# Kernel tuning notes

Measured on AMD Instinct MI355X. Metric: run time of the kernel, lower is better.

Reference implementation:

```python
import jax, jax.numpy as jnp
import numpy as np

L = 3          # num_layer
E_DIM = 64     # emb_dim
B = 4          # graphs per batch
N = 20000      # nodes per graph
E = 320000     # edges per graph
IN_DIM = 21    # raw node feature dim (Linear(21, emb_dim))
BN_EPS = 1e-5


def setup_inputs() -> dict:
    key = jax.random.key(0)
    ks = jax.random.split(key, 16)
    h2 = 2 * E_DIM
    inp = {
        "x": jax.random.normal(ks[0], (B, N, IN_DIM), dtype=jnp.float32),
        "edge_index": jax.random.randint(ks[1], (B, 2, E), 0, N, dtype=jnp.int64),
        "edge_attr": jax.random.normal(ks[2], (B, E, 1), dtype=jnp.float32),
        # layer-0 input node embedding Linear(21, emb)
        "inW": jax.random.normal(ks[3], (IN_DIM, E_DIM), dtype=jnp.float32) * 0.1,
        "inb": jnp.zeros((E_DIM,), dtype=jnp.float32),
        # per-layer edge encoder Linear(1, emb)
        "edgeW": jax.random.normal(ks[4], (L, 1, E_DIM), dtype=jnp.float32) * 0.1,
        "edgeb": jnp.zeros((L, E_DIM), dtype=jnp.float32),
        # per-layer MLP: Linear(2e,2e) -> BN(2e) -> ReLU -> Linear(2e,e)
        "W1": jax.random.normal(ks[5], (L, h2, h2), dtype=jnp.float32) * 0.05,
        "b1": jnp.zeros((L, h2), dtype=jnp.float32),
        "gamma": jnp.ones((L, h2), dtype=jnp.float32),
        "beta": jnp.zeros((L, h2), dtype=jnp.float32),
        "W2": jax.random.normal(ks[6], (L, h2, E_DIM), dtype=jnp.float32) * 0.05,
        "b2": jnp.zeros((L, E_DIM), dtype=jnp.float32),
    }
    return inp


def _batchnorm_train(h, g, b):
    # BatchNorm1d in training mode: per-graph stats over the node dim, biased var
    m = h.mean(axis=0)
    v = jnp.mean((h - m) ** 2, axis=0)
    return (h - m) * jax.lax.rsqrt(v + BN_EPS) * g + b


def _gin_layer(xg, eig, eag, W1l, b1l, gl, bel, W2l, b2l):
    # xg [N,e], eig [2,E], eag [E,e]
    x_j = xg[eig[0]]                                   # gather source nodes [E,e]
    msg = jnp.concatenate([x_j, eag], axis=-1)         # [E,2e]
    aggr = jax.ops.segment_sum(msg, eig[1], num_segments=N)  # scatter-add [N,2e]
    h = aggr @ W1l + b1l
    h = _batchnorm_train(h, gl, bel)
    h = jax.nn.relu(h)
    return h @ W2l + b2l                               # [N,e]


def reference(x, edge_index, edge_attr, inW, inb, edgeW, edgeb, W1, b1, gamma, beta, W2, b2):
    h = x
    for l in range(L):
        ea = edge_attr @ edgeW[l] + edgeb[l]           # [B,E,e] edge embeddings
        if l == 0:
            h = h @ inW + inb                          # [B,N,e]
        h = jax.vmap(_gin_layer, in_axes=(0, 0, 0, None, None, None, None, None, None))(
            h, edge_index, ea, W1[l], b1[l], gamma[l], beta[l], W2[l], b2[l])
        if l < L - 1:                                  # drop_ratio=0 -> dropout is identity
            h = jax.nn.relu(h)
    return h  # JK='last'
```

## Files before the change

### kernel.cpp

```cpp
#include <hip/hip_runtime.h>
#include <hip/hip_bf16.h>
#include <hip/hip_fp16.h>

#define NB 4
#define NN 20000
#define NE 320000
#define IND 21
#define ED 64
#define H2 128
#define CAP 48
#define NRANGE 32
#define RNODES 625
#define BINCAP 160
#define SCAP 11264
#define BN_EPS 1e-5f

typedef __attribute__((ext_vector_type(8))) short bf16x8;
typedef __attribute__((ext_vector_type(4))) float f32x4;

__device__ __forceinline__ short f2bf(float f) {
    unsigned u = __float_as_uint(f);
    u += 0x7fffu + ((u >> 16) & 1u);
    return (short)(u >> 16);
}

__device__ __forceinline__ void add8(float* ac, const uint4 rv) {
    const float2 f0 = __half22float2(*(const __half2*)&rv.x);
    const float2 f1 = __half22float2(*(const __half2*)&rv.y);
    const float2 f2 = __half22float2(*(const __half2*)&rv.z);
    const float2 f3 = __half22float2(*(const __half2*)&rv.w);
    ac[0] += f0.x; ac[1] += f0.y; ac[2] += f1.x; ac[3] += f1.y;
    ac[4] += f2.x; ac[5] += f2.y; ac[6] += f3.x; ac[7] += f3.y;
}


__global__ __launch_bounds__(256) void k_compact(
    const int* __restrict__ ei, const float* __restrict__ eattr,
    uint2* __restrict__ stage, int* __restrict__ rcnt)
{
    __shared__ uint2 bins[NRANGE][BINCAP];
    __shared__ int lcnt[NRANGE];
    __shared__ int lbase[NRANGE];
    const int b = blockIdx.y;
    const int e0 = blockIdx.x * 2048;
    const int tid = threadIdx.x;
    if (tid < NRANGE) lcnt[tid] = 0;
    __syncthreads();
    const int* srcp = ei + (size_t)b * 2 * NE;
    const int* dstp = srcp + NE;
    const float* ap = eattr + (size_t)b * NE;
    #pragma unroll
    for (int it = 0; it < 8; ++it) {
        const int e = e0 + it * 256 + tid;
        if (e < NE) {
            const int dst = dstp[e];
            const int src = srcp[e];
            const float a = ap[e];
            const int r = dst / RNODES;
            const unsigned lo = ((unsigned)src & 0xffffu) | (__float_as_uint(a) & 0xffff0000u);
            const int p = atomicAdd(&lcnt[r], 1);
            if (p < BINCAP) bins[r][p] = make_uint2(lo, (unsigned)dst);
        }
    }
    __syncthreads();
    if (tid < NRANGE) lbase[tid] = atomicAdd(&rcnt[b * NRANGE + tid], min(lcnt[tid], BINCAP));
    __syncthreads();
    for (int r = 0; r < NRANGE; ++r) {
        const int c = min(lcnt[r], BINCAP);
        uint2* dstg = stage + (size_t)(b * NRANGE + r) * SCAP + lbase[r];
        for (int i = tid; i < c; i += 256) dstg[i] = bins[r][i];
    }
}

__global__ __launch_bounds__(256) void k_scatter(
    const uint2* __restrict__ stage, const int* __restrict__ rcnt,
    int* __restrict__ cnt, unsigned int* __restrict__ bucket)
{
    const int b = blockIdx.x >> 5;
    const int g = blockIdx.x & 31;
    const int count = min(rcnt[b * NRANGE + g], SCAP);
    const uint2* st = stage + (size_t)(b * NRANGE + g) * SCAP;
    for (int idx = threadIdx.x; idx < count; idx += 256) {
        const uint2 rec = st[idx];
        const int node = b * NN + (int)rec.y;
        const int p = atomicAdd(&cnt[node], 1);
        if (p < CAP) bucket[(size_t)node * CAP + p] = rec.x;
    }
}

__global__ __launch_bounds__(256) void k_in(
    const float* __restrict__ x, const float* __restrict__ inW,
    const float* __restrict__ inb, __half* __restrict__ h)
{
    const int b = blockIdx.y;
    const int t = blockIdx.x * 256 + threadIdx.x;
    const int n = t >> 6;
    const int c = t & 63;
    if (n >= NN) return;
    const float* xr = x + ((size_t)b * NN + n) * IND;
    float acc = inb[c];
    #pragma unroll
    for (int k = 0; k < IND; ++k) acc += xr[k] * inW[k * ED + c];
    h[((size_t)b * NN + n) * ED + c] = __float2half(acc);
}

__global__ __launch_bounds__(256) void k_prep(
    const float* __restrict__ W1, const float* __restrict__ W2,
    const float* __restrict__ edgeW, const float* __restrict__ edgeb,
    short* __restrict__ W1T, short* __restrict__ W2T,
    float* __restrict__ uv_all, float* __restrict__ stats_all)
{
    const int l = blockIdx.x;
    const int tid = threadIdx.x;
    ((float4*)(stats_all + l * 1024))[tid] = make_float4(0.f, 0.f, 0.f, 0.f);
    for (int i = tid; i < H2 * ED; i += 256) {
        const int j = i >> 6, k = i & 63;
        W1T[l * 8192 + i] = f2bf(W1[(size_t)l * H2 * H2 + k * H2 + j]);
    }
    for (int i = tid; i < ED * H2; i += 256) {
        const int c = i >> 7, k = i & 127;
        W2T[l * 8192 + i] = f2bf(W2[(size_t)l * H2 * ED + k * ED + c]);
    }
    if (tid < H2) {
        float u = 0.f, v = 0.f;
        for (int k = 0; k < ED; ++k) {
            const float w = W1[(size_t)l * H2 * H2 + (ED + k) * H2 + tid];
            u += edgeW[l * ED + k] * w;
            v += edgeb[l * ED + k] * w;
        }
        uv_all[l * 256 + tid] = u;
        uv_all[l * 256 + H2 + tid] = v;
    }
}


__global__ __launch_bounds__(256, 4) void k_aggr_stats(
    const __half* __restrict__ h, const unsigned int* __restrict__ bucket,
    const int* __restrict__ cnt_arr, const short* __restrict__ W1Tl,
    const float* __restrict__ b1l, const float* __restrict__ uv_l,
    __half* __restrict__ h1g, float* __restrict__ stats_l)
{
    __shared__ short atb[16 * 72];
    __shared__ float sdl[16], ddl[16];
    __shared__ float uL[H2], vL[H2], bbL[H2];
    const int tid = threadIdx.x;
    const int g = blockIdx.x & 7;
    const int b = g >> 1;
    const int t = ((int)blockIdx.x >> 3) * 2 + (g & 1);
    const int n0 = t * 16;

    if (tid < H2) { uL[tid] = uv_l[tid]; vL[tid] = uv_l[H2 + tid]; bbL[tid] = b1l[tid]; }

    {
        const int node = n0 + (tid >> 4);
        const int sub = tid & 15;
        const int q = sub & 7;
        const int par = sub >> 3;
        const int cntraw = cnt_arr[b * NN + node];
        const int cnt = min(cntraw, CAP);
        const unsigned int* row = bucket + (size_t)(b * NN + node) * CAP;
        const __half* hp = h + (size_t)b * NN * ED + q * 8;
        float ac[8];
        #pragma unroll
        for (int i = 0; i < 8; ++i) ac[i] = 0.f;
        float sa = 0.f;
        const int nq = cnt >> 2;
        int qq = par;
        for (; qq + 2 < nq; qq += 4) {
            const uint4 sA = *(const uint4*)(row + qq * 4);
            const uint4 sB = *(const uint4*)(row + (qq + 2) * 4);
            const uint4 r0 = *(const uint4*)(hp + (size_t)(sA.x & 0xffffu) * ED);
            const uint4 r1 = *(const uint4*)(hp + (size_t)(sA.y & 0xffffu) * ED);
            const uint4 r2 = *(const uint4*)(hp + (size_t)(sA.z & 0xffffu) * ED);
            const uint4 r3 = *(const uint4*)(hp + (size_t)(sA.w & 0xffffu) * ED);
            const uint4 r4 = *(const uint4*)(hp + (size_t)(sB.x & 0xffffu) * ED);
            const uint4 r5 = *(const uint4*)(hp + (size_t)(sB.y & 0xffffu) * ED);
            const uint4 r6 = *(const uint4*)(hp + (size_t)(sB.z & 0xffffu) * ED);
            const uint4 r7 = *(const uint4*)(hp + (size_t)(sB.w & 0xffffu) * ED);
            sa += __uint_as_float(sA.x & 0xffff0000u) + __uint_as_float(sA.y & 0xffff0000u)
                + __uint_as_float(sA.z & 0xffff0000u) + __uint_as_float(sA.w & 0xffff0000u)
                + __uint_as_float(sB.x & 0xffff0000u) + __uint_as_float(sB.y & 0xffff0000u)
                + __uint_as_float(sB.z & 0xffff0000u) + __uint_as_float(sB.w & 0xffff0000u);
            add8(ac, r0); add8(ac, r1); add8(ac, r2); add8(ac, r3);
            add8(ac, r4); add8(ac, r5); add8(ac, r6); add8(ac, r7);
        }
        for (; qq < nq; qq += 2) {
            const uint4 sA = *(const uint4*)(row + qq * 4);
            const uint4 r0 = *(const uint4*)(hp + (size_t)(sA.x & 0xffffu) * ED);
            const uint4 r1 = *(const uint4*)(hp + (size_t)(sA.y & 0xffffu) * ED);
            const uint4 r2 = *(const uint4*)(hp + (size_t)(sA.z & 0xffffu) * ED);
            const uint4 r3 = *(const uint4*)(hp + (size_t)(sA.w & 0xffffu) * ED);
            sa += __uint_as_float(sA.x & 0xffff0000u) + __uint_as_float(sA.y & 0xffff0000u)
                + __uint_as_float(sA.z & 0xffff0000u) + __uint_as_float(sA.w & 0xffff0000u);
            add8(ac, r0); add8(ac, r1); add8(ac, r2); add8(ac, r3);
        }
        if ((nq & 1) == par) {
            for (int p = nq * 4; p < cnt; ++p) {
                const unsigned e = row[p];
                sa += __uint_as_float(e & 0xffff0000u);
                const uint4 r0 = *(const uint4*)(hp + (size_t)(e & 0xffffu) * ED);
                add8(ac, r0);
            }
        }
        #pragma unroll
        for (int i = 0; i < 8; ++i) ac[i] += __shfl_xor(ac[i], 8);
        sa += __shfl_xor(sa, 8);
        if (par == 0) {
            uint4 pk;
            pk.x = (unsigned short)f2bf(ac[0]) | ((unsigned int)(unsigned short)f2bf(ac[1]) << 16);
            pk.y = (unsigned short)f2bf(ac[2]) | ((unsigned int)(unsigned short)f2bf(ac[3]) << 16);
            pk.z = (unsigned short)f2bf(ac[4]) | ((unsigned int)(unsigned short)f2bf(ac[5]) << 16);
            pk.w = (unsigned short)f2bf(ac[6]) | ((unsigned int)(unsigned short)f2bf(ac[7]) << 16);
            *(uint4*)&atb[(tid >> 4) * 72 + q * 8] = pk;
            if (q == 0) {
                sdl[tid >> 4] = sa;
                ddl[tid >> 4] = (float)cntraw;
            }
        }
    }
    __syncthreads();

    const int l = tid & 63;
    const int w = tid >> 6;
    const int m = l & 15, quad = l >> 4;
    const int jb = w * 2;
    f32x4 acc[2];
    acc[0] = (f32x4){0.f, 0.f, 0.f, 0.f};
    acc[1] = (f32x4){0.f, 0.f, 0.f, 0.f};
    #pragma unroll
    for (int kc = 0; kc < 2; ++kc) {
        const bf16x8 fa = *(const bf16x8*)&atb[m * 72 + kc * 32 + quad * 8];
        #pragma unroll
        for (int t2 = 0; t2 < 2; ++t2) {
            const bf16x8 fb = *(const bf16x8*)&W1Tl[((jb + t2) * 16 + m) * 64 + kc * 32 + quad * 8];
            acc[t2] = __builtin_amdgcn_mfma_f32_16x16x32_bf16(fa, fb, acc[t2], 0, 0, 0);
        }
    }
    float sa_r[4], dg_r[4];
    #pragma unroll
    for (int r = 0; r < 4; ++r) {
        const int row = quad * 4 + r;
        sa_r[r] = sdl[row]; dg_r[r] = ddl[row];
    }
    #pragma unroll
    for (int t2 = 0; t2 < 2; ++t2) {
        const int j = (jb + t2) * 16 + m;
        const float u = uL[j], v = vL[j], bb = bbL[j];
        float ls = 0.f, lq = 0.f;
        #pragma unroll
        for (int r = 0; r < 4; ++r) {
            const float h1v = acc[t2][r] + sa_r[r] * u + dg_r[r] * v + bb;
            h1g[((size_t)b * NN + n0 + quad * 4 + r) * H2 + j] = __float2half(h1v);
            ls += h1v; lq += h1v * h1v;
        }
        ls += __shfl_xor(ls, 16); ls += __shfl_xor(ls, 32);
        lq += __shfl_xor(lq, 16); lq += __shfl_xor(lq, 32);
        if (l < 16) {
            atomicAdd(&stats_l[b * H2 + j], ls);
            atomicAdd(&stats_l[NB * H2 + b * H2 + j], lq);
        }
    }
}

__global__ __launch_bounds__(256) void k_mlp_out(
    const __half* __restrict__ h1g, const short* __restrict__ W2Tl,
    const float* __restrict__ stats_l, const float* __restrict__ gamma_l,
    const float* __restrict__ beta_l, const float* __restrict__ b2l,
    __half* __restrict__ outh, float* __restrict__ outf, int last)
{
    __shared__ short wt[ED * 136];
    __shared__ short pb[64 * 136];
    const int tid = threadIdx.x;
    const int g = blockIdx.x & 7;
    const int b = g >> 1;
    const int t = ((int)blockIdx.x >> 3) * 2 + (g & 1);
    if (t >= (NN + 63) / 64) return;
    const int n0 = t * 64;

    const uint4* h1p = (const uint4*)(h1g + ((size_t)b * NN + n0) * H2);
    const uint4 hv0 = h1p[tid];
    const uint4 hv1 = h1p[tid + 256];
    const uint4 hv2 = h1p[tid + 512];
    const uint4 hv3 = h1p[tid + 768];

    for (int i = tid; i < 1024; i += 256)
        *(uint4*)&wt[(i >> 4) * 136 + (i & 15) * 8] = ((const uint4*)W2Tl)[i];

    const int ch0 = (tid & 15) * 8;
    float sc[8], sh[8];
    #pragma unroll
    for (int e = 0; e < 8; ++e) {
        const int j = ch0 + e;
        const float mm = stats_l[b * H2 + j] * (1.f / NN);
        const float var = fmaxf(stats_l[NB * H2 + b * H2 + j] * (1.f / NN) - mm * mm, 0.f);
        const float rs = rsqrtf(var + BN_EPS);
        sc[e] = gamma_l[j] * rs;
        sh[e] = beta_l[j] - mm * sc[e];
    }

    {
        uint4 hv;
        short ob[8];
        #define BN8(K, HV)                                                    \
        {                                                                     \
            hv = HV;                                                          \
            const __half* hp = (const __half*)&hv;                            \
            _Pragma("unroll")                                                 \
            for (int e = 0; e < 8; ++e) {                                     \
                const float xv = __half2float(hp[e]);                         \
                ob[e] = f2bf(fmaxf(xv * sc[e] + sh[e], 0.f));                 \
            }                                                                 \
            *(uint4*)&pb[((tid >> 4) + (K) * 16) * 136 + ch0] = *(uint4*)ob;  \
        }
        BN8(0, hv0) BN8(1, hv1) BN8(2, hv2) BN8(3, hv3)
        #undef BN8
    }
    __syncthreads();

    {
        const int l = tid & 63;
        const int w = tid >> 6;
        const int m = l & 15, quad = l >> 4;
        f32x4 acc2[4];
        #pragma unroll
        for (int i = 0; i < 4; ++i) acc2[i] = (f32x4){0.f, 0.f, 0.f, 0.f};
        #pragma unroll
        for (int kc = 0; kc < 4; ++kc) {
            const bf16x8 fa = *(const bf16x8*)&pb[(w * 16 + m) * 136 + kc * 32 + quad * 8];
            #pragma unroll
            for (int t2 = 0; t2 < 4; ++t2) {
                const bf16x8 fb = *(const bf16x8*)&wt[(t2 * 16 + m) * 136 + kc * 32 + quad * 8];
                acc2[t2] = __builtin_amdgcn_mfma_f32_16x16x32_bf16(fa, fb, acc2[t2], 0, 0, 0);
            }
        }
        #pragma unroll
        for (int t2 = 0; t2 < 4; ++t2) {
            const int c = t2 * 16 + m;
            const float bb2 = b2l[c];
            #pragma unroll
            for (int r = 0; r < 4; ++r) {
                const int row = w * 16 + quad * 4 + r;
                const int n = n0 + row;
                if (n < NN) {
                    const size_t idx = ((size_t)b * NN + n) * ED + c;
                    float o = acc2[t2][r] + bb2;
                    if (last) outf[idx] = o;
                    else outh[idx] = __float2half(fmaxf(o, 0.f));
                }
            }
        }
    }
}


extern "C" void kernel_launch(void* const* d_in, const int* in_sizes, int n_in,
                              void* d_out, int out_size, void* d_ws, size_t ws_size,
                              hipStream_t stream) {
    const float* x     = (const float*)d_in[0];
    const int*   ei    = (const int*)d_in[1];
    const float* eattr = (const float*)d_in[2];
    const float* inW   = (const float*)d_in[3];
    const float* inb   = (const float*)d_in[4];
    const float* edgeW = (const float*)d_in[5];
    const float* edgeb = (const float*)d_in[6];
    const float* W1    = (const float*)d_in[7];
    const float* b1    = (const float*)d_in[8];
    const float* gamma = (const float*)d_in[9];
    const float* beta  = (const float*)d_in[10];
    const float* W2    = (const float*)d_in[11];
    const float* b2    = (const float*)d_in[12];
    float* out = (float*)d_out;

    int*   cnt    = (int*)d_ws;
    int*   rcnt   = cnt + NB * NN;
    uint2* stage  = (uint2*)(rcnt + 128);
    unsigned int* bucket = (unsigned int*)(stage + (size_t)NB * NRANGE * SCAP);
    __half* hh    = (__half*)(bucket + (size_t)NB * NN * CAP);
    __half* h1g   = hh + (size_t)NB * NN * ED;
    short* W1T    = (short*)(h1g + (size_t)NB * NN * H2);
    short* W2T    = W1T + 3 * 8192;
    float* uv_all = (float*)(W2T + 3 * 8192);
    float* stats  = uv_all + 3 * 256;

    hipMemsetAsync(cnt, 0, ((size_t)NB * NN + 128) * sizeof(int), stream);

    k_compact<<<dim3((NE + 2047) / 2048, NB), 256, 0, stream>>>(ei, eattr, stage, rcnt);
    k_scatter<<<NB * NRANGE, 256, 0, stream>>>(stage, rcnt, cnt, bucket);
    k_in<<<dim3(NN * ED / 256, NB), 256, 0, stream>>>(x, inW, inb, hh);
    k_prep<<<3, 256, 0, stream>>>(W1, W2, edgeW, edgeb, W1T, W2T, uv_all, stats);

    const int nblk1 = 8 * 625;
    const int nblk2 = 8 * (((NN + 63) / 64 + 1) / 2);
    for (int l = 0; l < 3; ++l) {
        k_aggr_stats<<<nblk1, 256, 0, stream>>>(hh, bucket, cnt,
            W1T + l * 8192, b1 + l * H2, uv_all + l * 256,
            h1g, stats + l * 1024);
        k_mlp_out<<<nblk2, 256, 0, stream>>>(h1g,
            W2T + l * 8192, stats + l * 1024,
            gamma + l * H2, beta + l * H2, b2 + l * ED,
            hh, out, (l == 2) ? 1 : 0);
    }
}
```

Measured before the change: 357.6 us.

## Split scatter ranges across more blocks and halve mlp_out node tile

The scatter kernel now launches four blocks per (graph, range) bin, each handling a quarter of the staged records, so 512 blocks run instead of 128. The output MLP kernel processes 32 nodes per block instead of 64, with each of the four waves computing a 16x32 output tile instead of 16x64, doubling the block count. Both changes aim to raise GPU occupancy and parallelism. The cost is that each mlp_out block reloads the W2 tile for half as much work, and the node bounds check is dropped because 20000 divides evenly by 32.

```diff
diff --git a/kernel.cpp b/kernel.cpp
--- a/kernel.cpp
+++ b/kernel.cpp
@@ -76,11 +76,15 @@
     const uint2* __restrict__ stage, const int* __restrict__ rcnt,
     int* __restrict__ cnt, unsigned int* __restrict__ bucket)
 {
-    const int b = blockIdx.x >> 5;
-    const int g = blockIdx.x & 31;
+    const int bg = blockIdx.x & 127;
+    const int seg = blockIdx.x >> 7;
+    const int b = bg >> 5;
+    const int g = bg & 31;
     const int count = min(rcnt[b * NRANGE + g], SCAP);
+    const int c0 = (count * seg) >> 2;
+    const int c1 = (count * (seg + 1)) >> 2;
     const uint2* st = stage + (size_t)(b * NRANGE + g) * SCAP;
-    for (int idx = threadIdx.x; idx < count; idx += 256) {
+    for (int idx = c0 + (int)threadIdx.x; idx < c1; idx += 256) {
         const uint2 rec = st[idx];
         const int node = b * NN + (int)rec.y;
         const int p = atomicAdd(&cnt[node], 1);
@@ -269,19 +273,17 @@
     __half* __restrict__ outh, float* __restrict__ outf, int last)
 {
     __shared__ short wt[ED * 136];
-    __shared__ short pb[64 * 136];
+    __shared__ short pb[32 * 136];
     const int tid = threadIdx.x;
     const int g = blockIdx.x & 7;
     const int b = g >> 1;
     const int t = ((int)blockIdx.x >> 3) * 2 + (g & 1);
-    if (t >= (NN + 63) / 64) return;
-    const int n0 = t * 64;
+    if (t >= 625) return;
+    const int n0 = t * 32;
 
     const uint4* h1p = (const uint4*)(h1g + ((size_t)b * NN + n0) * H2);
     const uint4 hv0 = h1p[tid];
     const uint4 hv1 = h1p[tid + 256];
-    const uint4 hv2 = h1p[tid + 512];
-    const uint4 hv3 = h1p[tid + 768];
 
     for (int i = tid; i < 1024; i += 256)
         *(uint4*)&wt[(i >> 4) * 136 + (i & 15) * 8] = ((const uint4*)W2Tl)[i];
@@ -312,7 +314,7 @@
             }                                                                 \
             *(uint4*)&pb[((tid >> 4) + (K) * 16) * 136 + ch0] = *(uint4*)ob;  \
         }
-        BN8(0, hv0) BN8(1, hv1) BN8(2, hv2) BN8(3, hv3)
+        BN8(0, hv0) BN8(1, hv1)
         #undef BN8
     }
     __syncthreads();
@@ -321,32 +323,31 @@
         const int l = tid & 63;
         const int w = tid >> 6;
         const int m = l & 15, quad = l >> 4;
-        f32x4 acc2[4];
-        #pragma unroll
-        for (int i = 0; i < 4; ++i) acc2[i] = (f32x4){0.f, 0.f, 0.f, 0.f};
+        const int mt = w & 1;
+        const int ntb = (w >> 1) * 2;
+        f32x4 acc2[2];
+        acc2[0] = (f32x4){0.f, 0.f, 0.f, 0.f};
+        acc2[1] = (f32x4){0.f, 0.f, 0.f, 0.f};
         #pragma unroll
         for (int kc = 0; kc < 4; ++kc) {
-            const bf16x8 fa = *(const bf16x8*)&pb[(w * 16 + m) * 136 + kc * 32 + quad * 8];
+            const bf16x8 fa = *(const bf16x8*)&pb[(mt * 16 + m) * 136 + kc * 32 + quad * 8];
             #pragma unroll
-            for (int t2 = 0; t2 < 4; ++t2) {
-                const bf16x8 fb = *(const bf16x8*)&wt[(t2 * 16 + m) * 136 + kc * 32 + quad * 8];
-                acc2[t2] = __builtin_amdgcn_mfma_f32_16x16x32_bf16(fa, fb, acc2[t2], 0, 0, 0);
+            for (int tt = 0; tt < 2; ++tt) {
+                const bf16x8 fb = *(const bf16x8*)&wt[((ntb + tt) * 16 + m) * 136 + kc * 32 + quad * 8];
+                acc2[tt] = __builtin_amdgcn_mfma_f32_16x16x32_bf16(fa, fb, acc2[tt], 0, 0, 0);
             }
         }
         #pragma unroll
-        for (int t2 = 0; t2 < 4; ++t2) {
-            const int c = t2 * 16 + m;
+        for (int tt = 0; tt < 2; ++tt) {
+            const int c = (ntb + tt) * 16 + m;
             const float bb2 = b2l[c];
             #pragma unroll
             for (int r = 0; r < 4; ++r) {
-                const int row = w * 16 + quad * 4 + r;
-                const int n = n0 + row;
-                if (n < NN) {
-                    const size_t idx = ((size_t)b * NN + n) * ED + c;
-                    float o = acc2[t2][r] + bb2;
-                    if (last) outf[idx] = o;
-                    else outh[idx] = __float2half(fmaxf(o, 0.f));
-                }
+                const int n = n0 + mt * 16 + quad * 4 + r;
+                const size_t idx = ((size_t)b * NN + n) * ED + c;
+                const float o = acc2[tt][r] + bb2;
+                if (last) outf[idx] = o;
+                else outh[idx] = __float2half(fmaxf(o, 0.f));
             }
         }
     }
@@ -385,12 +386,12 @@
     hipMemsetAsync(cnt, 0, ((size_t)NB * NN + 128) * sizeof(int), stream);
 
     k_compact<<<dim3((NE + 2047) / 2048, NB), 256, 0, stream>>>(ei, eattr, stage, rcnt);
-    k_scatter<<<NB * NRANGE, 256, 0, stream>>>(stage, rcnt, cnt, bucket);
+    k_scatter<<<4 * NB * NRANGE, 256, 0, stream>>>(stage, rcnt, cnt, bucket);
     k_in<<<dim3(NN * ED / 256, NB), 256, 0, stream>>>(x, inW, inb, hh);
     k_prep<<<3, 256, 0, stream>>>(W1, W2, edgeW, edgeb, W1T, W2T, uv_all, stats);
 
     const int nblk1 = 8 * 625;
-    const int nblk2 = 8 * (((NN + 63) / 64 + 1) / 2);
+    const int nblk2 = 8 * 313;
     for (int l = 0; l < 3; ++l) {
         k_aggr_stats<<<nblk1, 256, 0, stream>>>(hh, bucket, cnt,
             W1T + l * 8192, b1 + l * H2, uv_all + l * 256,
```

Measured after the change: 347.8 us. 1.03x faster.
